# Performance work log

Measured on AMD Instinct MI355X. Metric: run time of the kernel, lower is better.

## Reference

```python
import jax, jax.numpy as jnp
import numpy as np
from jax import lax

# ---- module hyperparameters (match init_kwargs) ----
FN_N, C, H, W = 4, 256, 160, 160      # x shape
HID, FC, R, AS = 256, 8, 4, 8         # hidden_depth, heads_count, downsample_size, anchor_size
SC = HID // FC                        # per-head depth (32)
S = AS * AS                           # anchors per head (64)
SCALE = float(C // FC) ** 0.5         # code uses sc = in_depth // heads for scaling
LN_EPS = 1e-5
NORM_EPS = 1e-12                      # F.normalize eps


def setup_inputs() -> dict:
    key = jax.random.key(0)
    ks = jax.random.split(key, 16)
    p = lambda i, shape: 0.02 * jax.random.normal(ks[i], shape, dtype=jnp.float32)
    return {
        "x": jax.random.normal(ks[0], (FN_N, C, H, W), dtype=jnp.float32),
        "w_down_qk": p(1, (C, 1, R, R)),   # depthwise conv, OIHW with groups=C
        "b_down_qk": p(2, (C,)),
        "ln_w": jnp.ones((C,), jnp.float32),
        "ln_b": jnp.zeros((C,), jnp.float32),
        "w_qk": p(3, (C, HID)), "b_qk": p(4, (HID,)),
        "w_v": p(5, (C, HID)), "b_v": p(6, (HID,)),
        "w_point": p(7, (C, HID)), "b_point": p(8, (HID,)),
        "down_alpha": jnp.ones((1,), jnp.float32),
        "down_beta": jnp.zeros((1,), jnp.float32),
        "alpha": jnp.ones((1,), jnp.float32),
        "beta": jnp.zeros((1,), jnp.float32),
        "w_m0": p(9, (HID, C)), "b_m0": p(10, (C,)),
        "w_m1": p(11, (HID, C)), "b_m1": p(12, (C,)),
    }


def _ln(t, w, b):
    mu = t.mean(-1, keepdims=True)
    var = ((t - mu) ** 2).mean(-1, keepdims=True)
    return (t - mu) / jnp.sqrt(var + LN_EPS) * w + b


def _l2n(t):
    return t / jnp.maximum(jnp.sqrt((t * t).sum(-1, keepdims=True)), NORM_EPS)


def _split(t):
    # '(fn n) h1 w1 (fp fc sc)' -> fp, (fn n fc), (h1 w1), sc
    N, Hh, Ww, _ = t.shape
    t = t.reshape(2, N // 2, Hh, Ww, 2, FC, SC).transpose(4, 0, 1, 5, 2, 3, 6)
    return t.reshape(2, N * FC, Hh * Ww, SC)


def _merge(t, N, Hh, Ww):
    # '(fn n fc) (h1 w1) sc' -> (fn n) h1 w1 (fc sc)
    return t.reshape(2, N // 2, FC, Hh, Ww, SC).transpose(0, 1, 3, 4, 2, 5).reshape(N, Hh, Ww, FC * SC)


def reference(x, w_down_qk, b_down_qk, ln_w, ln_b, w_qk, b_qk, w_v, b_v,
              w_point, b_point, down_alpha, down_beta, alpha, beta,
              w_m0, b_m0, w_m1, b_m1):
    N, Cc, h, w = x.shape
    sh, sw = h // R, w // R
    m, L = N * FC, sh * sw
    # --- downsample ---
    dq = lax.conv_general_dilated(x, w_down_qk, (R, R), 'VALID',
                                  feature_group_count=Cc,
                                  dimension_numbers=('NCHW', 'OIHW', 'NCHW'))
    dq = dq + b_down_qk[None, :, None, None]
    dv = x.reshape(N, Cc, sh, R, sw, R).max(axis=(3, 5))  # MaxPool2d(R, R)
    dq = _ln(dq.transpose(0, 2, 3, 1), ln_w, ln_b) @ w_qk + b_qk  # (N,sh,sw,HID)
    dv = _ln(dv.transpose(0, 2, 3, 1), ln_w, ln_b) @ w_v + b_v
    dcat = jnp.concatenate([dq, dv], axis=-1)                     # (N,sh,sw,2*HID)
    # --- anchor proposal: adaptive avg pool (sh divisible by AS -> block mean) ---
    kh, kw = sh // AS, sw // AS
    anc = dcat.reshape(N, AS, kh, AS, kw, 2 * HID).mean(axis=(2, 4))
    dqk, dvv = _split(dcat)   # (m, L, SC) each
    aqk, avv = _split(anc)    # (m, S, SC) each
    # --- downsampled cross-attention between the two feature sets ---
    half = m // 2
    sim = jnp.einsum('nld,nsd->nls', dqk[:half], dqk[half:]) / SCALE
    att01 = jnp.nan_to_num(jax.nn.softmax(sim, axis=2))
    att10 = jnp.nan_to_num(jax.nn.softmax(sim.transpose(0, 2, 1), axis=2))
    msg0 = jnp.einsum('nls,nsd->nld', att01, dvv[half:])
    msg1 = jnp.einsum('nsl,nld->nsd', att10, dvv[:half])
    att_msg = jnp.concatenate([msg0, msg1], axis=0)               # (m, L, SC)
    att_msg = (_merge(att_msg, N, sh, sw) @ w_m0 + b_m0).transpose(0, 3, 1, 2)
    att_message = jax.image.resize(att_msg, (N, Cc, h, w), 'bilinear')
    # --- top-1 anchor routing + index_add scatter aggregation ---
    sims = jax.nn.sigmoid(down_alpha * jnp.einsum('mlc,msc->mls', _l2n(dqk), _l2n(aqk)) + down_beta)
    vals = sims.max(axis=2)
    idx = jnp.argmax(sims, axis=2)
    idx_flat = (idx + S * jnp.arange(m)[:, None]).reshape(-1)
    dflat = jnp.concatenate([dqk, dvv], axis=2).reshape(m * L, 2 * SC)
    aflat = jnp.concatenate([aqk, avv], axis=2).reshape(m * S, 2 * SC)
    dflat = jnp.concatenate([dflat, jnp.ones((m * L, 1), dflat.dtype)], axis=1)
    aflat = jnp.concatenate([aflat, jnp.ones((m * S, 1), aflat.dtype)], axis=1)
    agg = aflat.at[idx_flat].add(vals.reshape(-1)[:, None] * dflat)
    aggregated = agg[:, :-1] / agg[:, -1:]                        # (m*S, 2*SC)
    # --- full-resolution point features ---
    xp = x.transpose(0, 2, 3, 1) @ w_point + b_point              # (N,h,w,HID)
    xp = xp.reshape(2, N // 2, h, w, FC, SC).transpose(0, 1, 4, 2, 3, 5).reshape(m, h * w, SC)
    # swap the two feature sets' clusters, split into point/value halves
    hr = m * S // 2
    aggregated = jnp.concatenate([aggregated[hr:], aggregated[:hr]], axis=0)
    agg2 = aggregated.reshape(2, N // 2, FC, S, 2, SC).transpose(4, 0, 1, 2, 3, 5).reshape(2, m, S, SC)
    ap, av = agg2[0], agg2[1]
    sims2 = jax.nn.sigmoid(alpha * jnp.einsum('mlc,msc->mls', _l2n(xp), _l2n(ap)) + beta)
    vals2 = sims2.max(axis=2)
    idx2 = jnp.argmax(sims2, axis=2)
    idx2_flat = (idx2 + S * jnp.arange(m)[:, None]).reshape(-1)
    disp = vals2.reshape(-1)[:, None] * av.reshape(m * S, SC)[idx2_flat]  # gather dispatch
    coc = disp.reshape(2, N // 2, FC, h, w, SC).transpose(0, 1, 3, 4, 2, 5).reshape(N, h, w, HID)
    coc_message = (coc @ w_m1 + b_m1).transpose(0, 3, 1, 2)
    return jnp.concatenate([att_message, coc_message], axis=1)    # (N, 2*C, h, w)
```

## Files before the change

### kernel.cpp

```cpp
#include <hip/hip_runtime.h>
#include <math.h>

#define CN 4
#define CC 256
#define CH 160
#define CW 160
#define SHH 40
#define SWW 40
#define CL 1600
#define CSC 32
#define CS 64
#define NHEAD 32
#define INV_SCALE 0.17677669529663687f

__device__ __forceinline__ int head_batch(int h) { return ((h >> 4) << 1) | ((h >> 3) & 1); }

__device__ __forceinline__ float norm32_np(const float* t)
{
    float lane[8];
    #pragma unroll
    for (int j = 0; j < 8; ++j) {
        float s = __fmul_rn(t[j], t[j]);
        s = __fadd_rn(s, __fmul_rn(t[j + 8], t[j + 8]));
        s = __fadd_rn(s, __fmul_rn(t[j + 16], t[j + 16]));
        s = __fadd_rn(s, __fmul_rn(t[j + 24], t[j + 24]));
        lane[j] = s;
    }
    float p01 = __fadd_rn(lane[0], lane[1]);
    float p23 = __fadd_rn(lane[2], lane[3]);
    float p45 = __fadd_rn(lane[4], lane[5]);
    float p67 = __fadd_rn(lane[6], lane[7]);
    return __fadd_rn(__fadd_rn(p01, p23), __fadd_rn(p45, p67));
}

__global__ __launch_bounds__(256)
void k_conv_pool(const float* __restrict__ x, const float* __restrict__ wdw,
                 const float* __restrict__ bdw,
                 float* __restrict__ dqn, float* __restrict__ dvn)
{
    int pix = blockIdx.x;
    int c = threadIdx.x;
    int n = pix / CL;
    int r = pix - n * CL;
    int oh = r / SWW;
    int ow = r - oh * SWW;
    const float* xp = x + ((long)(n * CC + c) * CH + oh * 4) * CW + ow * 4;
    float4 w0 = *(const float4*)(wdw + c * 16);
    float4 w1 = *(const float4*)(wdw + c * 16 + 4);
    float4 w2 = *(const float4*)(wdw + c * 16 + 8);
    float4 w3 = *(const float4*)(wdw + c * 16 + 12);
    float4 r0 = *(const float4*)(xp);
    float4 r1 = *(const float4*)(xp + CW);
    float4 r2 = *(const float4*)(xp + 2 * CW);
    float4 r3 = *(const float4*)(xp + 3 * CW);
    float conv = r0.x * w0.x + r0.y * w0.y + r0.z * w0.z + r0.w * w0.w
               + r1.x * w1.x + r1.y * w1.y + r1.z * w1.z + r1.w * w1.w
               + r2.x * w2.x + r2.y * w2.y + r2.z * w2.z + r2.w * w2.w
               + r3.x * w3.x + r3.y * w3.y + r3.z * w3.z + r3.w * w3.w;
    conv += bdw[c];
    float mx = fmaxf(fmaxf(fmaxf(r0.x, r0.y), fmaxf(r0.z, r0.w)),
               fmaxf(fmaxf(fmaxf(r1.x, r1.y), fmaxf(r1.z, r1.w)),
               fmaxf(fmaxf(fmaxf(r2.x, r2.y), fmaxf(r2.z, r2.w)),
                     fmaxf(fmaxf(r3.x, r3.y), fmaxf(r3.z, r3.w)))));
    dqn[(long)pix * CC + c] = conv;
    dvn[(long)pix * CC + c] = mx;
}

__global__ __launch_bounds__(256)
void k_ln(float* __restrict__ b0, float* __restrict__ b1,
          const float* __restrict__ lnw, const float* __restrict__ lnb)
{
    float* buf = blockIdx.y ? b1 : b0;
    int row = blockIdx.x;
    int c = threadIdx.x;
    float v = buf[(long)row * CC + c];
    float s = v, s2 = v * v;
    #pragma unroll
    for (int off = 32; off >= 1; off >>= 1) {
        s += __shfl_xor(s, off);
        s2 += __shfl_xor(s2, off);
    }
    __shared__ float red[8];
    int wid = c >> 6, lane = c & 63;
    if (lane == 0) { red[wid * 2] = s; red[wid * 2 + 1] = s2; }
    __syncthreads();
    float ts = 0.f, ts2 = 0.f;
    #pragma unroll
    for (int w = 0; w < 4; ++w) { ts += red[w * 2]; ts2 += red[w * 2 + 1]; }
    float mu = ts * (1.0f / 256.0f);
    float var = ts2 * (1.0f / 256.0f) - mu * mu;
    float rstd = 1.0f / sqrtf(var + 1e-5f);
    buf[(long)row * CC + c] = (v - mu) * rstd * lnw[c] + lnb[c];
}

#define GBK 16
#define GSTR 68
__global__ __launch_bounds__(256)
void k_gemm256(const float* __restrict__ A, const float* __restrict__ Wt,
               const float* __restrict__ bias, float* __restrict__ Cout,
               int M, int amode, int aplane,
               int omode, int oplane, long obstride, int ocoff)
{
    __shared__ float As[GBK][GSTR];
    __shared__ float Bs[GBK][GSTR];
    const int t = threadIdx.x;
    const int m0 = blockIdx.x * 64;
    const int n0 = blockIdx.y * 64;
    const int ty = t >> 4, tx = t & 15;
    float acc[4][4] = {};
    long abase = 0; int p0 = 0;
    if (amode == 1) {
        int nb = m0 / aplane;
        p0 = m0 - nb * aplane;
        abase = (long)nb * 256 * aplane;
    }
    for (int k0 = 0; k0 < 256; k0 += GBK) {
        if (amode == 0) {
            int i = t >> 2, j4 = (t & 3) * 4;
            float4 a = *(const float4*)(A + (long)(m0 + i) * 256 + k0 + j4);
            As[j4 + 0][i] = a.x; As[j4 + 1][i] = a.y;
            As[j4 + 2][i] = a.z; As[j4 + 3][i] = a.w;
        } else {
            int j = t >> 4, i4 = (t & 15) * 4;
            float4 a = *(const float4*)(A + abase + (long)(k0 + j) * aplane + p0 + i4);
            *(float4*)&As[j][i4] = a;
        }
        {
            int k = t >> 4, n4 = (t & 15) * 4;
            float4 b = *(const float4*)(Wt + (long)(k0 + k) * 256 + n0 + n4);
            *(float4*)&Bs[k][n4] = b;
        }
        __syncthreads();
        #pragma unroll
        for (int k = 0; k < GBK; ++k) {
            float4 a = *(const float4*)&As[k][ty * 4];
            float4 b = *(const float4*)&Bs[k][tx * 4];
            float aa[4] = {a.x, a.y, a.z, a.w};
            float bb[4] = {b.x, b.y, b.z, b.w};
            #pragma unroll
            for (int ii = 0; ii < 4; ++ii)
                #pragma unroll
                for (int jj = 0; jj < 4; ++jj)
                    acc[ii][jj] = fmaf(aa[ii], bb[jj], acc[ii][jj]);
        }
        __syncthreads();
    }
    int colb = n0 + tx * 4;
    float4 bi = *(const float4*)(bias + colb);
    float bias4[4] = {bi.x, bi.y, bi.z, bi.w};
    if (omode == 0) {
        #pragma unroll
        for (int ii = 0; ii < 4; ++ii) {
            long mrow = m0 + ty * 4 + ii;
            float4 o;
            o.x = acc[ii][0] + bias4[0];
            o.y = acc[ii][1] + bias4[1];
            o.z = acc[ii][2] + bias4[2];
            o.w = acc[ii][3] + bias4[3];
            *(float4*)(Cout + mrow * 256 + colb) = o;
        }
    } else {
        int nb2 = m0 / oplane;
        #pragma unroll
        for (int ii = 0; ii < 4; ++ii) {
            int mrow = m0 + ty * 4 + ii;
            int p = mrow - nb2 * oplane;
            #pragma unroll
            for (int jj = 0; jj < 4; ++jj)
                Cout[(long)nb2 * obstride + (long)(ocoff + colb + jj) * oplane + p]
                    = acc[ii][jj] + bias4[jj];
        }
    }
}

__global__ __launch_bounds__(256)
void k_anchor(const float* __restrict__ dq, const float* __restrict__ dv,
              float* __restrict__ ancq, float* __restrict__ ancv)
{
    int bs = blockIdx.x;
    int c = threadIdx.x;
    int b = bs >> 6, s = bs & 63;
    int ai = s >> 3, aj = s & 7;
    float colq[5], colv[5];
    #pragma unroll
    for (int dj = 0; dj < 5; ++dj) {
        long pix0 = (long)b * CL + (ai * 5) * SWW + aj * 5 + dj;
        float cq = dq[pix0 * CC + c];
        float cv = dv[pix0 * CC + c];
        #pragma unroll
        for (int di = 1; di < 5; ++di) {
            long pix = pix0 + (long)di * SWW;
            cq = __fadd_rn(cq, dq[pix * CC + c]);
            cv = __fadd_rn(cv, dv[pix * CC + c]);
        }
        colq[dj] = cq; colv[dj] = cv;
    }
    float sq = colq[0], sv = colv[0];
    #pragma unroll
    for (int dj = 1; dj < 5; ++dj) {
        sq = __fadd_rn(sq, colq[dj]);
        sv = __fadd_rn(sv, colv[dj]);
    }
    ancq[(long)bs * CC + c] = sq / 25.0f;
    ancv[(long)bs * CC + c] = sv / 25.0f;
}

__global__ __launch_bounds__(256)
void k_attn(const float* __restrict__ dq, const float* __restrict__ dv,
            float* __restrict__ att4)
{
    __shared__ float Kl[64][36];
    __shared__ float Vl[64][36];
    int qt = blockIdx.x;
    int h = blockIdx.y;
    int b = head_batch(h), fc = h & 7;
    int pb = b ^ 2;
    int t = threadIdx.x;
    int qi = t >> 3, part = t & 7;
    int lane = t & 63;
    int qrow = qt * 32 + qi;

    float qreg[32];
    {
        const float4* qp = (const float4*)(dq + (long)(b * CL + qrow) * CC + fc * CSC);
        #pragma unroll
        for (int j8 = 0; j8 < 8; ++j8) {
            float4 f = qp[j8];
            qreg[4 * j8 + 0] = f.x; qreg[4 * j8 + 1] = f.y;
            qreg[4 * j8 + 2] = f.z; qreg[4 * j8 + 3] = f.w;
        }
    }
    float Oa[4] = {0, 0, 0, 0};
    float mrun = -INFINITY, lrun = 0.f;

    for (int kt = 0; kt < 25; ++kt) {
        {
            int li = t >> 2, lp = t & 3;
            const float* kp = dq + (long)(pb * CL + kt * 64 + li) * CC + fc * CSC + lp * 8;
            const float* vp = dv + (long)(pb * CL + kt * 64 + li) * CC + fc * CSC + lp * 8;
            *(float4*)&Kl[li][lp * 8]     = *(const float4*)kp;
            *(float4*)&Kl[li][lp * 8 + 4] = *(const float4*)(kp + 4);
            *(float4*)&Vl[li][lp * 8]     = *(const float4*)vp;
            *(float4*)&Vl[li][lp * 8 + 4] = *(const float4*)(vp + 4);
        }
        __syncthreads();
        float sc[8];
        float tmax = -INFINITY;
        #pragma unroll
        for (int si = 0; si < 8; ++si) {
            int s = si * 8 + part;
            const float4* kr = (const float4*)&Kl[s][0];
            float d0 = 0.f;
            #pragma unroll
            for (int j8 = 0; j8 < 8; ++j8) {
                float4 k4 = kr[j8];
                d0 = fmaf(qreg[4 * j8 + 0], k4.x, d0);
                d0 = fmaf(qreg[4 * j8 + 1], k4.y, d0);
                d0 = fmaf(qreg[4 * j8 + 2], k4.z, d0);
                d0 = fmaf(qreg[4 * j8 + 3], k4.w, d0);
            }
            d0 *= INV_SCALE;
            sc[si] = d0;
            tmax = fmaxf(tmax, d0);
        }
        tmax = fmaxf(tmax, __shfl_xor(tmax, 1));
        tmax = fmaxf(tmax, __shfl_xor(tmax, 2));
        tmax = fmaxf(tmax, __shfl_xor(tmax, 4));
        float mnew = fmaxf(mrun, tmax);
        float corr = expf(mrun - mnew);
        float wexp[8];
        float psum = 0.f;
        #pragma unroll
        for (int si = 0; si < 8; ++si) {
            wexp[si] = expf(sc[si] - mnew);
            psum += wexp[si];
        }
        psum += __shfl_xor(psum, 1);
        psum += __shfl_xor(psum, 2);
        psum += __shfl_xor(psum, 4);
        lrun = lrun * corr + psum;
        #pragma unroll
        for (int j = 0; j < 4; ++j) Oa[j] *= corr;
        int lbase = lane & ~7;
        #pragma unroll
        for (int si = 0; si < 8; ++si) {
            #pragma unroll
            for (int p8 = 0; p8 < 8; ++p8) {
                int s = si * 8 + p8;
                float w = __shfl(wexp[si], lbase | p8, 64);
                const float4 v4 = *(const float4*)&Vl[s][part * 4];
                Oa[0] = fmaf(w, v4.x, Oa[0]);
                Oa[1] = fmaf(w, v4.y, Oa[1]);
                Oa[2] = fmaf(w, v4.z, Oa[2]);
                Oa[3] = fmaf(w, v4.w, Oa[3]);
            }
        }
        mrun = mnew;
        __syncthreads();
    }
    float inv = 1.0f / lrun;
    float* op = att4 + (long)(b * CL + qrow) * CC + fc * CSC + part * 4;
    float4 o;
    o.x = Oa[0] * inv; o.y = Oa[1] * inv; o.z = Oa[2] * inv; o.w = Oa[3] * inv;
    *(float4*)op = o;
}

__global__ __launch_bounds__(256)
void k_resize(const float* __restrict__ am, float* __restrict__ out)
{
    int plane = blockIdx.y;
    int o = blockIdx.x * 256 + threadIdx.x;
    int y = o / CW, xx = o - y * CW;
    const float* src = am + (long)plane * (SHH * SWW);
    float fy = (y + 0.5f) * 0.25f - 0.5f;
    int iy0 = (int)floorf(fy);
    float wy = fy - iy0;
    int iy1 = min(iy0 + 1, SHH - 1); iy0 = max(iy0, 0);
    float fx = (xx + 0.5f) * 0.25f - 0.5f;
    int ix0 = (int)floorf(fx);
    float wx = fx - ix0;
    int ix1 = min(ix0 + 1, SWW - 1); ix0 = max(ix0, 0);
    float v00 = src[iy0 * SWW + ix0], v01 = src[iy0 * SWW + ix1];
    float v10 = src[iy1 * SWW + ix0], v11 = src[iy1 * SWW + ix1];
    float v = (1.f - wy) * ((1.f - wx) * v00 + wx * v01)
            + wy * ((1.f - wx) * v10 + wx * v11);
    int n = plane >> 8, c = plane & 255;
    out[((long)(n * 512 + c)) * (CH * CW) + o] = v;
}

__global__ __launch_bounds__(64)
void k_aqkn_np(const float* __restrict__ ancq, float* __restrict__ aqkn)
{
    int h = blockIdx.x, s = threadIdx.x;
    int b = head_batch(h), fc = h & 7;
    const float* p = ancq + (long)(b * CS + s) * CC + fc * CSC;
    float a[32];
    #pragma unroll
    for (int d = 0; d < 32; ++d) a[d] = p[d];
    float anorm = fmaxf(sqrtf(norm32_np(a)), 1e-12f);
    #pragma unroll
    for (int d = 0; d < 32; ++d) aqkn[(long)(h * CS + s) * CSC + d] = a[d] / anorm;
}

__global__ __launch_bounds__(256)
void k_routing1_lite(const float* __restrict__ dq, const float* __restrict__ aqkn,
                     const float* __restrict__ dalpha, const float* __restrict__ dbeta,
                     float* __restrict__ valb, int* __restrict__ idxb)
{
    __shared__ float An[CS * CSC];
    int h = blockIdx.y;
    int b = head_batch(h), fc = h & 7;
    int t = threadIdx.x;
    for (int u = t; u < CS * CSC; u += 256) An[u] = aqkn[(long)h * CS * CSC + u];
    __syncthreads();
    int l = blockIdx.x * 256 + t;
    if (l >= CL) return;
    float da = dalpha[0], db = dbeta[0];
    const float* qp = dq + (long)(b * CL + l) * CC + fc * CSC;
    float q[32];
    #pragma unroll
    for (int d = 0; d < 32; ++d) q[d] = qp[d];
    float qnorm = fmaxf(sqrtf(norm32_np(q)), 1e-12f);
    float qn[32];
    #pragma unroll
    for (int d = 0; d < 32; ++d) qn[d] = q[d] / qnorm;
    float best = -1.f; int bi = 0;
    for (int sg = 0; sg < CS; sg += 4) {
        float acc[4];
        #pragma unroll
        for (int i = 0; i < 4; ++i) {
            const float4 a0 = *(const float4*)&An[(sg + i) * CSC];
            acc[i] = __fmul_rn(qn[0], a0.x);
            acc[i] = __fadd_rn(acc[i], __fmul_rn(qn[1], a0.y));
            acc[i] = __fadd_rn(acc[i], __fmul_rn(qn[2], a0.z));
            acc[i] = __fadd_rn(acc[i], __fmul_rn(qn[3], a0.w));
        }
        #pragma unroll
        for (int dg = 1; dg < 8; ++dg) {
            #pragma unroll
            for (int i = 0; i < 4; ++i) {
                const float4 a4 = *(const float4*)&An[(sg + i) * CSC + dg * 4];
                acc[i] = __fadd_rn(acc[i], __fmul_rn(qn[4 * dg + 0], a4.x));
                acc[i] = __fadd_rn(acc[i], __fmul_rn(qn[4 * dg + 1], a4.y));
                acc[i] = __fadd_rn(acc[i], __fmul_rn(qn[4 * dg + 2], a4.z));
                acc[i] = __fadd_rn(acc[i], __fmul_rn(qn[4 * dg + 3], a4.w));
            }
        }
        #pragma unroll
        for (int i = 0; i < 4; ++i) {
            float tv = __fadd_rn(__fmul_rn(da, acc[i]), db);
            float sim = 1.0f / (1.0f + expf(-tv));
            if (sim > best) { best = sim; bi = sg + i; }
        }
    }
    valb[h * CL + l] = best;
    idxb[h * CL + l] = bi;
}

__global__ __launch_bounds__(64)
void k_scatter(const float* __restrict__ dq, const float* __restrict__ dv,
               const float* __restrict__ ancq, const float* __restrict__ ancv,
               const float* __restrict__ valb, const int* __restrict__ idxb,
               float* __restrict__ agg)
{
    int cl = blockIdx.x;
    int h = cl >> 6, s = cl & 63;
    int b = head_batch(h), fc = h & 7;
    int j = threadIdx.x;
    const float* base = (j < 32) ? (dq + (long)b * CL * CC + fc * CSC + j)
                                 : (dv + (long)b * CL * CC + fc * CSC + (j - 32));
    float init = (j < 32) ? ancq[(long)(b * CS + s) * CC + fc * CSC + j]
                          : ancv[(long)(b * CS + s) * CC + fc * CSC + (j - 32)];
    float acc = init, cnt = 1.0f;
    const int* ix = idxb + h * CL;
    const float* vb = valb + h * CL;
    for (int l = 0; l < CL; ++l) {
        if (ix[l] == s) {
            float v = vb[l];
            acc = __fadd_rn(acc, __fmul_rn(v, base[(long)l * CC]));
            cnt = __fadd_rn(cnt, v);
        }
    }
    agg[(long)cl * 65 + j] = acc;
    if (j == 0) agg[(long)cl * 65 + 64] = cnt;
}

__global__ __launch_bounds__(64)
void k_finalize(const float* __restrict__ agg, float* __restrict__ apn,
                float* __restrict__ avo)
{
    int h = blockIdx.x, s = threadIdx.x;
    int sh_ = h ^ 16;
    const float* r = agg + (long)(sh_ * CS + s) * 65;
    float cnt = r[64];
    float a[32];
    #pragma unroll
    for (int d = 0; d < 32; ++d) a[d] = r[d] / cnt;
    float nrm = fmaxf(sqrtf(norm32_np(a)), 1e-12f);
    long o = (long)(h * CS + s) * CSC;
    #pragma unroll
    for (int d = 0; d < 32; ++d) {
        apn[o + d] = a[d] / nrm;
        avo[o + d] = r[32 + d] / cnt;
    }
}

__global__ __launch_bounds__(512)
void k_routing2_lite(float* __restrict__ xp, const float* __restrict__ apn,
                     const float* __restrict__ avv,
                     const float* __restrict__ alpha_, const float* __restrict__ beta_)
{
    __shared__ float Anl[16384];
    int blk = blockIdx.x;
    int b = blk / 400;
    int p0 = (blk % 400) * 64;
    int t = threadIdx.x;
    int pi = t >> 3, fc = t & 7;
    int p = p0 + pi;
    int hb0 = ((b >> 1) << 4) | ((b & 1) << 3);
    float al = alpha_[0], be = beta_[0];
    for (int u = t; u < 16384; u += 512) {
        int fci = u >> 11, s = (u >> 5) & 63, d = u & 31;
        Anl[((s * 8 + (d >> 2)) * 8 + fci) * 4 + (d & 3)] = apn[(long)hb0 * 2048 + u];
    }
    __syncthreads();
    float* xr = xp + ((long)b * 25600 + p) * CC + fc * CSC;
    float q[32];
    #pragma unroll
    for (int j8 = 0; j8 < 8; ++j8) {
        float4 f = ((const float4*)xr)[j8];
        q[4 * j8 + 0] = f.x; q[4 * j8 + 1] = f.y;
        q[4 * j8 + 2] = f.z; q[4 * j8 + 3] = f.w;
    }
    float qnorm = fmaxf(sqrtf(norm32_np(q)), 1e-12f);
    float qn[32];
    #pragma unroll
    for (int d = 0; d < 32; ++d) qn[d] = q[d] / qnorm;

    float best = -1.f; int bi = 0;
    for (int sg = 0; sg < CS; sg += 4) {
        float acc[4];
        #pragma unroll
        for (int i = 0; i < 4; ++i) {
            const float4 a0 = *(const float4*)&Anl[(((sg + i) * 8 + 0) * 8 + fc) * 4];
            acc[i] = __fmul_rn(qn[0], a0.x);
            acc[i] = __fadd_rn(acc[i], __fmul_rn(qn[1], a0.y));
            acc[i] = __fadd_rn(acc[i], __fmul_rn(qn[2], a0.z));
            acc[i] = __fadd_rn(acc[i], __fmul_rn(qn[3], a0.w));
        }
        #pragma unroll
        for (int dg = 1; dg < 8; ++dg) {
            #pragma unroll
            for (int i = 0; i < 4; ++i) {
                const float4 a4 = *(const float4*)&Anl[(((sg + i) * 8 + dg) * 8 + fc) * 4];
                acc[i] = __fadd_rn(acc[i], __fmul_rn(qn[4 * dg + 0], a4.x));
                acc[i] = __fadd_rn(acc[i], __fmul_rn(qn[4 * dg + 1], a4.y));
                acc[i] = __fadd_rn(acc[i], __fmul_rn(qn[4 * dg + 2], a4.z));
                acc[i] = __fadd_rn(acc[i], __fmul_rn(qn[4 * dg + 3], a4.w));
            }
        }
        #pragma unroll
        for (int i = 0; i < 4; ++i) {
            float tv = __fadd_rn(__fmul_rn(al, acc[i]), be);
            float sim = 1.0f / (1.0f + expf(-tv));
            if (sim > best) { best = sim; bi = sg + i; }
        }
    }
    const float* av = avv + ((long)(hb0 + fc) * CS + bi) * CSC;
    #pragma unroll
    for (int d = 0; d < 32; ++d) xr[d] = __fmul_rn(best, av[d]);
}

extern "C" void kernel_launch(void* const* d_in, const int* in_sizes, int n_in,
                              void* d_out, int out_size, void* d_ws, size_t ws_size,
                              hipStream_t stream)
{
    const float* x      = (const float*)d_in[0];
    const float* wdw    = (const float*)d_in[1];
    const float* bdw    = (const float*)d_in[2];
    const float* lnw    = (const float*)d_in[3];
    const float* lnb    = (const float*)d_in[4];
    const float* wqk    = (const float*)d_in[5];
    const float* bqk    = (const float*)d_in[6];
    const float* wv     = (const float*)d_in[7];
    const float* bv     = (const float*)d_in[8];
    const float* wpoint = (const float*)d_in[9];
    const float* bpoint = (const float*)d_in[10];
    const float* dalpha = (const float*)d_in[11];
    const float* dbeta  = (const float*)d_in[12];
    const float* alpha_ = (const float*)d_in[13];
    const float* beta_  = (const float*)d_in[14];
    const float* wm0    = (const float*)d_in[15];
    const float* bm0    = (const float*)d_in[16];
    const float* wm1    = (const float*)d_in[17];
    const float* bm1    = (const float*)d_in[18];
    float* out = (float*)d_out;
    float* ws = (float*)d_ws;

    float* dqn  = ws;
    float* dvn  = ws + 1638400;
    float* dq   = ws + 3276800;
    float* dv   = ws + 4915200;
    float* ancq = ws + 6553600;
    float* ancv = ws + 6619136;
    float* aqkn = ws + 6684672;
    float* agg  = ws + 6750208;
    float* apn  = ws + 6883328;
    float* avv  = ws + 6948864;
    float* valb = ws + 7014400;
    int*   idxb = (int*)(ws + 7065600);
    float* xp   = ws + 7116800;
    float* att4 = dqn;
    float* am   = dvn;

    k_conv_pool<<<dim3(CN * CL), dim3(256), 0, stream>>>(x, wdw, bdw, dqn, dvn);
    k_ln<<<dim3(CN * CL, 2), dim3(256), 0, stream>>>(dqn, dvn, lnw, lnb);
    k_gemm256<<<dim3(100, 4), dim3(256), 0, stream>>>(dqn, wqk, bqk, dq, 6400, 0, 0, 0, 0, 0, 0);
    k_gemm256<<<dim3(100, 4), dim3(256), 0, stream>>>(dvn, wv,  bv,  dv, 6400, 0, 0, 0, 0, 0, 0);
    k_anchor<<<dim3(CN * CS), dim3(256), 0, stream>>>(dq, dv, ancq, ancv);

    k_attn<<<dim3(50, NHEAD), dim3(256), 0, stream>>>(dq, dv, att4);
    k_gemm256<<<dim3(100, 4), dim3(256), 0, stream>>>(att4, wm0, bm0, am, 6400, 0, 0,
                                                      1, 1600, 409600L, 0);
    k_resize<<<dim3(100, CN * 256), dim3(256), 0, stream>>>(am, out);

    k_aqkn_np<<<dim3(NHEAD), dim3(64), 0, stream>>>(ancq, aqkn);
    k_routing1_lite<<<dim3(7, NHEAD), dim3(256), 0, stream>>>(dq, aqkn, dalpha, dbeta,
                                                              valb, idxb);
    k_scatter<<<dim3(2048), dim3(64), 0, stream>>>(dq, dv, ancq, ancv, valb, idxb, agg);
    k_finalize<<<dim3(NHEAD), dim3(64), 0, stream>>>(agg, apn, avv);
    k_gemm256<<<dim3(1600, 4), dim3(256), 0, stream>>>(x, wpoint, bpoint, xp, 102400,
                                                       1, 25600, 0, 0, 0, 0);
    k_routing2_lite<<<dim3(1600), dim3(512), 0, stream>>>(xp, apn, avv, alpha_, beta_);
    k_gemm256<<<dim3(1600, 4), dim3(256), 0, stream>>>(xp, wm1, bm1, out, 102400, 0, 0,
                                                       1, 25600, 13107200L, 256);
}
```

Before: 1.227 ms.

## Use bf16 MFMA for final coc projection and prefetch K/V in attention

Replaces the final fp32 GEMM (coc @ w_m1) with a bf16 MFMA kernel that converts activations to bf16 on load and uses a pre-transposed bf16 copy of w_m1, writing output in channel-major layout. The attention kernel also prefetches the next K/V tile into registers while the current tile is computed. The bf16 conversion lowers precision of a large GEMM, which risks tolerance failures, and adds a small weight-transpose kernel per call.

```diff
diff --git a/kernel.cpp b/kernel.cpp
--- a/kernel.cpp
+++ b/kernel.cpp
@@ -13,7 +13,17 @@
 #define NHEAD 32
 #define INV_SCALE 0.17677669529663687f
 
+typedef __attribute__((ext_vector_type(8))) short bf16x8;
+typedef __attribute__((ext_vector_type(4))) float f32x4;
+
 __device__ __forceinline__ int head_batch(int h) { return ((h >> 4) << 1) | ((h >> 3) & 1); }
+
+__device__ __forceinline__ short f2bf(float f)
+{
+    unsigned u = __float_as_uint(f);
+    u += 0x7FFFu + ((u >> 16) & 1u);
+    return (short)(u >> 16);
+}
 
 __device__ __forceinline__ float norm32_np(const float* t)
 {
@@ -233,17 +243,27 @@
     float Oa[4] = {0, 0, 0, 0};
     float mrun = -INFINITY, lrun = 0.f;
 
+    int li = t >> 2, lp = t & 3;
+    float4 kA, kB, vA, vB;
+    {
+        const float* kp = dq + (long)(pb * CL + li) * CC + fc * CSC + lp * 8;
+        const float* vp = dv + (long)(pb * CL + li) * CC + fc * CSC + lp * 8;
+        kA = *(const float4*)kp; kB = *(const float4*)(kp + 4);
+        vA = *(const float4*)vp; vB = *(const float4*)(vp + 4);
+    }
+
     for (int kt = 0; kt < 25; ++kt) {
-        {
-            int li = t >> 2, lp = t & 3;
-            const float* kp = dq + (long)(pb * CL + kt * 64 + li) * CC + fc * CSC + lp * 8;
-            const float* vp = dv + (long)(pb * CL + kt * 64 + li) * CC + fc * CSC + lp * 8;
-            *(float4*)&Kl[li][lp * 8]     = *(const float4*)kp;
-            *(float4*)&Kl[li][lp * 8 + 4] = *(const float4*)(kp + 4);
-            *(float4*)&Vl[li][lp * 8]     = *(const float4*)vp;
-            *(float4*)&Vl[li][lp * 8 + 4] = *(const float4*)(vp + 4);
-        }
+        *(float4*)&Kl[li][lp * 8]     = kA;
+        *(float4*)&Kl[li][lp * 8 + 4] = kB;
+        *(float4*)&Vl[li][lp * 8]     = vA;
+        *(float4*)&Vl[li][lp * 8 + 4] = vB;
         __syncthreads();
+        if (kt + 1 < 25) {
+            const float* kp = dq + (long)(pb * CL + (kt + 1) * 64 + li) * CC + fc * CSC + lp * 8;
+            const float* vp = dv + (long)(pb * CL + (kt + 1) * 64 + li) * CC + fc * CSC + lp * 8;
+            kA = *(const float4*)kp; kB = *(const float4*)(kp + 4);
+            vA = *(const float4*)vp; vB = *(const float4*)(vp + 4);
+        }
         float sc[8];
         float tmax = -INFINITY;
         #pragma unroll
@@ -509,6 +529,67 @@
     const float* av = avv + ((long)(hb0 + fc) * CS + bi) * CSC;
     #pragma unroll
     for (int d = 0; d < 32; ++d) xr[d] = __fmul_rn(best, av[d]);
+}
+
+__global__ __launch_bounds__(256)
+void k_wm1t_bf16(const float* __restrict__ wm1, short* __restrict__ wt)
+{
+    int n = blockIdx.x;
+    int k = threadIdx.x;
+    wt[n * 256 + k] = f2bf(wm1[k * 256 + n]);
+}
+
+__global__ __launch_bounds__(256)
+void k_gemm_bf16_final(const float* __restrict__ coc, const short* __restrict__ wt,
+                       const float* __restrict__ bias, float* __restrict__ out)
+{
+    __shared__ short As[64][40];
+    __shared__ short Bs[64][40];
+    const int t = threadIdx.x;
+    const int m0 = blockIdx.x * 64;
+    const int n0 = blockIdx.y * 64;
+    const int nb = m0 / 25600;
+    const int p0 = m0 - nb * 25600;
+    const int w = t >> 6;
+    const int l = t & 63;
+    const int lr = l & 15, lk = l >> 4;
+
+    f32x4 acc[4] = {};
+    for (int k0 = 0; k0 < 256; k0 += 32) {
+        {
+            int row = t >> 2, kq = (t & 3) * 8;
+            const float* ap = coc + (long)(m0 + row) * 256 + k0 + kq;
+            float4 a1 = *(const float4*)ap;
+            float4 a2 = *(const float4*)(ap + 4);
+            bf16x8 v;
+            v[0] = f2bf(a1.x); v[1] = f2bf(a1.y); v[2] = f2bf(a1.z); v[3] = f2bf(a1.w);
+            v[4] = f2bf(a2.x); v[5] = f2bf(a2.y); v[6] = f2bf(a2.z); v[7] = f2bf(a2.w);
+            *(bf16x8*)&As[row][kq] = v;
+        }
+        {
+            int col = t >> 2, kq = (t & 3) * 8;
+            bf16x8 v = *(const bf16x8*)&wt[(n0 + col) * 256 + k0 + kq];
+            *(bf16x8*)&Bs[col][kq] = v;
+        }
+        __syncthreads();
+        bf16x8 af = *(const bf16x8*)&As[w * 16 + lr][lk * 8];
+        #pragma unroll
+        for (int c = 0; c < 4; ++c) {
+            bf16x8 bfv = *(const bf16x8*)&Bs[c * 16 + lr][lk * 8];
+            acc[c] = __builtin_amdgcn_mfma_f32_16x16x32_bf16(af, bfv, acc[c], 0, 0, 0);
+        }
+        __syncthreads();
+    }
+    #pragma unroll
+    for (int c = 0; c < 4; ++c) {
+        int col = n0 + c * 16 + lr;
+        float bv = bias[col];
+        #pragma unroll
+        for (int r = 0; r < 4; ++r) {
+            int p = p0 + w * 16 + lk * 4 + r;
+            out[(long)nb * 13107200 + (long)(256 + col) * 25600 + p] = acc[c][r] + bv;
+        }
+    }
 }
 
 extern "C" void kernel_launch(void* const* d_in, const int* in_sizes, int n_in,
@@ -549,7 +630,8 @@
     float* avv  = ws + 6948864;
     float* valb = ws + 7014400;
     int*   idxb = (int*)(ws + 7065600);
-    float* xp   = ws + 7116800;
+    short* wt   = (short*)(ws + 7116800);
+    float* xp   = ws + 7149568;
     float* att4 = dqn;
     float* am   = dvn;
 
@@ -572,6 +654,6 @@
     k_gemm256<<<dim3(1600, 4), dim3(256), 0, stream>>>(x, wpoint, bpoint, xp, 102400,
                                                        1, 25600, 0, 0, 0, 0);
     k_routing2_lite<<<dim3(1600), dim3(512), 0, stream>>>(xp, apn, avv, alpha_, beta_);
-    k_gemm256<<<dim3(1600, 4), dim3(256), 0, stream>>>(xp, wm1, bm1, out, 102400, 0, 0,
-                                                       1, 25600, 13107200L, 256);
-}
+    k_wm1t_bf16<<<dim3(256), dim3(256), 0, stream>>>(wm1, wt);
+    k_gemm_bf16_final<<<dim3(1600, 4), dim3(256), 0, stream>>>(xp, wt, bm1, out);
+}
```

Result: faster. 1.051 ms (-14.4%).
